# Kernel optimization log

Hardware: AMD Instinct MI355X
Metric: run time of the kernel (lower is better)

The kernel has to match this reference:

```python
import jax, jax.numpy as jnp
import numpy as np

NUM_ADAPTIVE = 8
WEIGHT_ALPHA = 1.0


def setup_inputs() -> dict:
    key = jax.random.key(0)
    k1, k2, k3, k4 = jax.random.split(key, 4)
    B, C, S = 128, 4, 65536
    inp = jax.random.normal(k1, (B, C, S), dtype=jnp.float32)
    target = jax.random.randint(k2, (B, S), 0, C, dtype=jnp.int64)
    adaptive_target = jax.random.randint(k3, (B, S), 0, NUM_ADAPTIVE, dtype=jnp.int64)
    mask = jax.random.randint(k4, (B, S), 0, 2).astype(jnp.float32)
    return {"input": inp, "target": target, "adaptive_target": adaptive_target, "mask": mask}


def reference(input, target, adaptive_target, mask):
    # Per-position cross entropy, reduction='none'. input: (B, C, S)
    logp = jax.nn.log_softmax(input, axis=1)                      # (B, C, S)
    ce = -jnp.take_along_axis(logp, target[:, None, :], axis=1)[:, 0, :]  # (B, S)

    loss = ce * mask                                              # masked per-position loss
    valid = (mask > 0).astype(loss.dtype)                         # (B, S)

    # Per-adaptive-class masked mean loss via a single segment reduction
    seg = adaptive_target.reshape(-1).astype(jnp.int32)
    class_sum = jax.ops.segment_sum((loss * valid).reshape(-1), seg, num_segments=NUM_ADAPTIVE)
    class_cnt = jax.ops.segment_sum(valid.reshape(-1), seg, num_segments=NUM_ADAPTIVE)

    fallback = jnp.mean(loss)                                     # loss.mean() in the original
    has = class_cnt > 0
    class_losses = jnp.where(has, class_sum / jnp.where(has, class_cnt, 1.0), fallback)
    class_counts = jnp.where(has, class_cnt, 1.0)

    total = jnp.sum(class_losses * class_counts)
    props = jnp.where(total > 0,
                      class_losses * class_counts / jnp.where(total > 0, total, 1.0),
                      jnp.full((NUM_ADAPTIVE,), 1.0 / NUM_ADAPTIVE, dtype=loss.dtype))
    class_weights = 1.0 + WEIGHT_ALPHA * props                    # (8,)

    adaptive_weights = class_weights[adaptive_target]             # gather back to (B, S)
    final_loss = jnp.sum(loss * adaptive_weights) / jnp.sum(mask)
    return final_loss
```

## Files before the change

### kernel.cpp

```cpp
#include <hip/hip_runtime.h>

constexpr int B = 128;
constexpr int C = 4;
constexpr int S = 65536;
constexpr int N = B * S;
constexpr int NG = N / 4;
constexpr int NSEG = 8;
constexpr int NACC = 2 * NSEG + 1;

__global__ __launch_bounds__(256) void ce_partial_kernel(
    const float* __restrict__ input,
    const int*   __restrict__ target,
    const int*   __restrict__ seg,
    const float* __restrict__ mask,
    float* __restrict__ acc)
{
    float ssum[NSEG], scnt[NSEG];
#pragma unroll
    for (int k = 0; k < NSEG; ++k) { ssum[k] = 0.f; scnt[k] = 0.f; }
    float msum = 0.f;

    const int stride = gridDim.x * blockDim.x;
    for (int g = blockIdx.x * blockDim.x + threadIdx.x; g < NG; g += stride) {
        const int p = g << 2;
        const int b = p >> 16;
        const int s = p & (S - 1);
        const int base = (b << 18) + s;

        const float4 l0 = *(const float4*)(input + base);
        const float4 l1 = *(const float4*)(input + base + S);
        const float4 l2 = *(const float4*)(input + base + 2 * S);
        const float4 l3 = *(const float4*)(input + base + 3 * S);
        const int4   tg = *(const int4*)(target + p);
        const int4   sv = *(const int4*)(seg + p);
        const float4 mk = *(const float4*)(mask + p);

        const float a0[4] = { l0.x, l0.y, l0.z, l0.w };
        const float a1[4] = { l1.x, l1.y, l1.z, l1.w };
        const float a2[4] = { l2.x, l2.y, l2.z, l2.w };
        const float a3[4] = { l3.x, l3.y, l3.z, l3.w };
        const int   tgv[4] = { tg.x, tg.y, tg.z, tg.w };
        const int   sgv[4] = { sv.x, sv.y, sv.z, sv.w };
        const float mkv[4] = { mk.x, mk.y, mk.z, mk.w };

#pragma unroll
        for (int j = 0; j < 4; ++j) {
            const float x0 = a0[j], x1 = a1[j], x2 = a2[j], x3 = a3[j];
            const float m = fmaxf(fmaxf(x0, x1), fmaxf(x2, x3));
            const float sum = __expf(x0 - m) + __expf(x1 - m)
                            + __expf(x2 - m) + __expf(x3 - m);
            const float lse = m + __logf(sum);
            const int t = tgv[j];
            const float chosen = (t == 0) ? x0 : (t == 1) ? x1 : (t == 2) ? x2 : x3;
            const float mval = mkv[j];
            const float loss = (lse - chosen) * mval;
            const float v = (mval > 0.f) ? 1.f : 0.f;
            const int sgj = sgv[j];
            msum += mval;
#pragma unroll
            for (int k = 0; k < NSEG; ++k) {
                const bool hit = (sgj == k);
                ssum[k] += hit ? loss : 0.f;
                scnt[k] += hit ? v : 0.f;
            }
        }
    }

    float vals[NACC];
#pragma unroll
    for (int k = 0; k < NSEG; ++k) { vals[k] = ssum[k]; vals[NSEG + k] = scnt[k]; }
    vals[16] = msum;
#pragma unroll
    for (int i = 0; i < NACC; ++i) {
        float v = vals[i];
#pragma unroll
        for (int off = 32; off > 0; off >>= 1)
            v += __shfl_xor(v, off, 64);
        vals[i] = v;
    }

    __shared__ float red[4][NACC];
    const int wave = threadIdx.x >> 6;
    const int lane = threadIdx.x & 63;
    if (lane == 0) {
#pragma unroll
        for (int i = 0; i < NACC; ++i) red[wave][i] = vals[i];
    }
    __syncthreads();
    if (threadIdx.x < NACC) {
        const int i = threadIdx.x;
        const float v = red[0][i] + red[1][i] + red[2][i] + red[3][i];
        atomicAdd(&acc[i], v);
    }
}

__global__ void ce_final_kernel(const float* __restrict__ acc, float* __restrict__ out)
{
    if (threadIdx.x != 0 || blockIdx.x != 0) return;

    float ssum[NSEG], scnt[NSEG];
    float tot_loss = 0.f;
    for (int k = 0; k < NSEG; ++k) {
        ssum[k] = acc[k];
        scnt[k] = acc[NSEG + k];
        tot_loss += ssum[k];
    }
    const float msum = acc[16];
    const float fallback = tot_loss / (float)N;

    float cl[NSEG], cc[NSEG];
    float total = 0.f;
    for (int k = 0; k < NSEG; ++k) {
        const bool has = scnt[k] > 0.f;
        cl[k] = has ? (ssum[k] / scnt[k]) : fallback;
        cc[k] = has ? scnt[k] : 1.f;
        total += cl[k] * cc[k];
    }
    float num = 0.f;
    for (int k = 0; k < NSEG; ++k) {
        const float prop = (total > 0.f) ? (cl[k] * cc[k] / total) : (1.f / (float)NSEG);
        const float w = 1.f + prop;
        num += w * ssum[k];
    }
    out[0] = num / msum;
}

extern "C" void kernel_launch(void* const* d_in, const int* in_sizes, int n_in,
                              void* d_out, int out_size, void* d_ws, size_t ws_size,
                              hipStream_t stream) {
    const float* input  = (const float*)d_in[0];
    const int*   target = (const int*)d_in[1];
    const int*   seg    = (const int*)d_in[2];
    const float* mask   = (const float*)d_in[3];
    float* acc = (float*)d_ws;
    float* out = (float*)d_out;

    hipMemsetAsync(d_ws, 0, NACC * sizeof(float), stream);
    ce_partial_kernel<<<2048, 256, 0, stream>>>(input, target, seg, mask, acc);
    ce_final_kernel<<<1, 64, 0, stream>>>(acc, out);
}
```

Before: 264.1 us.

## Replace atomic accumulation with per-block partials and unroll fixed-trip loop

Each block now writes its 17 partial sums to a per-block slot in workspace rather than issuing global atomicAdds, and a 1024-thread final kernel reduces these partials with shuffles and shared memory. This removes the memset launch and contention on the 17 accumulator addresses. The grid-stride loop also becomes a compile-time trip count with full unrolling, so the compiler can issue more loads ahead. The cost is more workspace traffic and a heavier final kernel, and the kernel now assumes the exact problem size.

After: 267.2 us. About the same (+1.2%).

```diff
diff --git a/kernel.cpp b/kernel.cpp
--- a/kernel.cpp
+++ b/kernel.cpp
@@ -8,20 +8,28 @@
 constexpr int NSEG = 8;
 constexpr int NACC = 2 * NSEG + 1;
 
-__global__ __launch_bounds__(256) void ce_partial_kernel(
+constexpr int GRID = 2048;
+constexpr int BLOCK = 256;
+constexpr int ITERS = NG / (GRID * BLOCK);
+static_assert(ITERS * GRID * BLOCK == NG, "grid must tile NG exactly");
+
+
+__global__ __launch_bounds__(BLOCK) void ce_partial_kernel(
     const float* __restrict__ input,
     const int*   __restrict__ target,
     const int*   __restrict__ seg,
     const float* __restrict__ mask,
-    float* __restrict__ acc)
+    float* __restrict__ pt)
 {
     float ssum[NSEG], scnt[NSEG];
 #pragma unroll
     for (int k = 0; k < NSEG; ++k) { ssum[k] = 0.f; scnt[k] = 0.f; }
     float msum = 0.f;
 
-    const int stride = gridDim.x * blockDim.x;
-    for (int g = blockIdx.x * blockDim.x + threadIdx.x; g < NG; g += stride) {
+    const int tid = blockIdx.x * BLOCK + threadIdx.x;
+#pragma unroll
+    for (int it = 0; it < ITERS; ++it) {
+        const int g = tid + it * (GRID * BLOCK);
         const int p = g << 2;
         const int b = p >> 16;
         const int s = p & (S - 1);
@@ -89,40 +97,68 @@
     __syncthreads();
     if (threadIdx.x < NACC) {
         const int i = threadIdx.x;
-        const float v = red[0][i] + red[1][i] + red[2][i] + red[3][i];
-        atomicAdd(&acc[i], v);
+        pt[i * GRID + blockIdx.x] =
+            red[0][i] + red[1][i] + red[2][i] + red[3][i];
     }
 }
 
-__global__ void ce_final_kernel(const float* __restrict__ acc, float* __restrict__ out)
+__global__ __launch_bounds__(1024) void ce_final_kernel(
+    const float* __restrict__ pt, float* __restrict__ out)
 {
-    if (threadIdx.x != 0 || blockIdx.x != 0) return;
+    const int t = threadIdx.x;
+    float vals[NACC];
+#pragma unroll
+    for (int i = 0; i < NACC; ++i) {
+        vals[i] = pt[i * GRID + t] + pt[i * GRID + t + 1024];
+#pragma unroll
+        for (int off = 32; off > 0; off >>= 1)
+            vals[i] += __shfl_xor(vals[i], off, 64);
+    }
 
-    float ssum[NSEG], scnt[NSEG];
-    float tot_loss = 0.f;
-    for (int k = 0; k < NSEG; ++k) {
-        ssum[k] = acc[k];
-        scnt[k] = acc[NSEG + k];
-        tot_loss += ssum[k];
+    __shared__ float red[16][NACC];
+    const int wave = t >> 6;
+    const int lane = t & 63;
+    if (lane == 0) {
+#pragma unroll
+        for (int i = 0; i < NACC; ++i) red[wave][i] = vals[i];
     }
-    const float msum = acc[16];
-    const float fallback = tot_loss / (float)N;
+    __syncthreads();
 
-    float cl[NSEG], cc[NSEG];
-    float total = 0.f;
-    for (int k = 0; k < NSEG; ++k) {
-        const bool has = scnt[k] > 0.f;
-        cl[k] = has ? (ssum[k] / scnt[k]) : fallback;
-        cc[k] = has ? scnt[k] : 1.f;
-        total += cl[k] * cc[k];
+    if (t == 0) {
+        float acc[NACC];
+        for (int i = 0; i < NACC; ++i) {
+            float v = 0.f;
+            for (int w = 0; w < 16; ++w) v += red[w][i];
+            acc[i] = v;
+        }
+
+        float ssum[NSEG], scnt[NSEG];
+        float tot_loss = 0.f;
+        for (int k = 0; k < NSEG; ++k) {
+            ssum[k] = acc[k];
+            scnt[k] = acc[NSEG + k];
+            tot_loss += ssum[k];
+        }
+        const float msum = acc[16];
+        const float fallback = tot_loss / (float)N;
+
+        float cl[NSEG], cc[NSEG];
+        float total = 0.f;
+        for (int k = 0; k < NSEG; ++k) {
+            const bool has = scnt[k] > 0.f;
+            cl[k] = has ? (ssum[k] / scnt[k]) : fallback;
+            cc[k] = has ? scnt[k] : 1.f;
+            total += cl[k] * cc[k];
+        }
+        float num = 0.f;
+        for (int k = 0; k < NSEG; ++k) {
+            const float prop = (total > 0.f) ? (cl[k] * cc[k] / total)
+                                             : (1.f / (float)NSEG);
+            const float w = 1.f + prop;
+            num += w * ssum[k];
+        }
+        out[0] = num / msum;
     }
-    float num = 0.f;
-    for (int k = 0; k < NSEG; ++k) {
-        const float prop = (total > 0.f) ? (cl[k] * cc[k] / total) : (1.f / (float)NSEG);
-        const float w = 1.f + prop;
-        num += w * ssum[k];
-    }
-    out[0] = num / msum;
 }
 
 extern "C" void kernel_launch(void* const* d_in, const int* in_sizes, int n_in,
@@ -132,10 +168,9 @@
     const int*   target = (const int*)d_in[1];
     const int*   seg    = (const int*)d_in[2];
     const float* mask   = (const float*)d_in[3];
-    float* acc = (float*)d_ws;
+    float* pt  = (float*)d_ws;
     float* out = (float*)d_out;
 
-    hipMemsetAsync(d_ws, 0, NACC * sizeof(float), stream);
-    ce_partial_kernel<<<2048, 256, 0, stream>>>(input, target, seg, mask, acc);
-    ce_final_kernel<<<1, 64, 0, stream>>>(acc, out);
+    ce_partial_kernel<<<GRID, BLOCK, 0, stream>>>(input, target, seg, mask, pt);
+    ce_final_kernel<<<1, 1024, 0, stream>>>(pt, out);
 }
```
